# Kernel tuning notes

Hardware: AMD Instinct MI355X
Metric: run time of the kernel (lower is better)

## Reference

```python
import jax, jax.numpy as jnp
import numpy as np

NUM_FRAMES = 6
HEADS = 16
DIM_HEAD = 64


def setup_inputs() -> dict:
    key = jax.random.key(0)
    ks = jax.random.split(key, 7)
    D = 1024
    x = jax.random.normal(ks[0], (12, 1024, D), dtype=jnp.float32)
    context = jax.random.normal(ks[1], (2, 1024, D), dtype=jnp.float32)
    s = 1.0 / np.sqrt(D)
    Wq = jax.random.normal(ks[2], (D, D), dtype=jnp.float32) * s
    Wk = jax.random.normal(ks[3], (D, D), dtype=jnp.float32) * s
    Wv = jax.random.normal(ks[4], (D, D), dtype=jnp.float32) * s
    Wo = jax.random.normal(ks[5], (D, D), dtype=jnp.float32) * s
    bo = jnp.zeros((D,), dtype=jnp.float32)
    return {"x": x, "context": context, "Wq": Wq, "Wk": Wk, "Wv": Wv, "Wo": Wo, "bo": bo}


def reference(x, context, Wq, Wk, Wv, Wo, bo):
    B, S, D = x.shape  # B=12, S=1024, D=1024
    scale = DIM_HEAD ** (-0.5)
    ab = B // NUM_FRAMES  # actual batch after frame inflation
    xr = x.reshape(ab, NUM_FRAMES * S, D)  # [ab, 6144, D]
    # Linear projections (torch Linear: y = x @ W.T)
    q = xr @ Wq.T            # [ab, Sq, inner]
    k = context @ Wk.T       # [ab, Sk, inner]
    v = context @ Wv.T
    Sq = q.shape[1]
    Sk = k.shape[1]
    q = q.reshape(ab, Sq, HEADS, DIM_HEAD).transpose(0, 2, 1, 3)  # [ab,h,Sq,d]
    k = k.reshape(ab, Sk, HEADS, DIM_HEAD).transpose(0, 2, 1, 3)
    v = v.reshape(ab, Sk, HEADS, DIM_HEAD).transpose(0, 2, 1, 3)
    attn = jnp.einsum("bhqd,bhkd->bhqk", q, k) * scale
    attn = jax.nn.softmax(attn, axis=-1)
    out = jnp.einsum("bhqk,bhkd->bhqd", attn, v)
    out = out.transpose(0, 2, 1, 3).reshape(ab, Sq, HEADS * DIM_HEAD)
    out = out @ Wo.T + bo  # dropout is identity at p=0 / eval
    return out.reshape(B, S, D)
```

## Files before the change

kernel.cpp:

```cpp
#include <hip/hip_runtime.h>

typedef short bf16x8 __attribute__((ext_vector_type(8)));
typedef float floatx4 __attribute__((ext_vector_type(4)));
typedef unsigned short u16;
typedef unsigned int u32;

__device__ __forceinline__ u16 f2bf(float f) {
  u32 u = __float_as_uint(f);
  u += 0x7FFF + ((u >> 16) & 1);
  return (u16)(u >> 16);
}
__device__ __forceinline__ u32 packbf(float a, float b) {
  return (u32)f2bf(a) | ((u32)f2bf(b) << 16);
}
__device__ __forceinline__ u32 permpack(u32 a_bits, u32 b_bits) {
  return __builtin_amdgcn_perm(b_bits, a_bits, 0x07060302u);
}

__device__ __forceinline__ float ex2(float x) {
#if __has_builtin(__builtin_amdgcn_exp2f)
  return __builtin_amdgcn_exp2f(x);
#else
  float r;
  asm("v_exp_f32 %0, %1" : "=v"(r) : "v"(x));
  return r;
#endif
}

__device__ __forceinline__ void gload_lds16(const u16* g, u16* l) {
  __builtin_amdgcn_global_load_lds(
      (const __attribute__((address_space(1))) void*)(const void*)g,
      (__attribute__((address_space(3))) void*)(void*)l, 16, 0, 0);
}

__device__ __forceinline__ int xcd_swz(int disp, int nwg) {
  const int q = nwg >> 3;
  return (disp & 7) * q + (disp >> 3);
}

__device__ __forceinline__ void bb_mainloop(const u16* __restrict__ A,
                                            const u16* __restrict__ W,
                                            u16* As, u16* Ws, int m0, int n0,
                                            floatx4 acc[4][4]) {
  const int tid = threadIdx.x, lane = tid & 63, w = tid >> 6;
  const int wm = w & 1, wn = w >> 1;
  const int m16 = lane & 15, quad = lane >> 4;
  const int lr = lane >> 2;
  const int sc = (lane & 3) * 8;

  const u16* Ag = A + (size_t)(m0 + w * 32 + lr) * 1024 + sc;
  const u16* Wg = W + (size_t)(n0 + w * 32 + lr) * 1024 + sc;
  u16* const Asl = &As[(w * 32) * 32];
  u16* const Wsl = &Ws[(w * 32) * 32];

#pragma unroll
  for (int i = 0; i < 4; ++i)
#pragma unroll
    for (int j = 0; j < 4; ++j) acc[i][j] = (floatx4)0.0f;

  for (int kt = 0; kt < 32; ++kt) {
    gload_lds16(Ag, Asl);
    gload_lds16(Ag + 16 * 1024, Asl + 16 * 32);
    gload_lds16(Wg, Wsl);
    gload_lds16(Wg + 16 * 1024, Wsl + 16 * 32);
    Ag += 32;
    Wg += 32;
    __syncthreads();
    bf16x8 af[4], bfr[4];
#pragma unroll
    for (int t = 0; t < 4; ++t) {
      af[t]  = *(const bf16x8*)&As[(wm * 64 + t * 16 + m16) * 32 + quad * 8];
      bfr[t] = *(const bf16x8*)&Ws[(wn * 64 + t * 16 + m16) * 32 + quad * 8];
    }
#pragma unroll
    for (int i = 0; i < 4; ++i)
#pragma unroll
      for (int j = 0; j < 4; ++j)
        acc[i][j] = __builtin_amdgcn_mfma_f32_16x16x32_bf16(af[i], bfr[j],
                                                            acc[i][j], 0, 0, 0);
    __syncthreads();
  }
}

__global__ __launch_bounds__(256) void gemm_qkv(
    const u16* __restrict__ xb, const u16* __restrict__ ctxb,
    const u16* __restrict__ wqb, const u16* __restrict__ wkb,
    const u16* __restrict__ wvb, u16* __restrict__ Qb, u16* __restrict__ Kbuf,
    u16* __restrict__ Vtb) {
  __shared__ u16 As[128 * 32];
  __shared__ u16 Ws[128 * 32];
  const int lane = threadIdx.x & 63, w = threadIdx.x >> 6;
  const int wm = w & 1, wn = w >> 1;
  const int m16 = lane & 15, quad = lane >> 4;
  const int disp = blockIdx.y * 8 + blockIdx.x;
  const int work = xcd_swz(disp, 1024);
  const int y = work >> 3;
  const int n0 = (work & 7) * 128;
  const u16 *A, *W;
  int m0, mode;
  if (y < 96)       { A = xb;   W = wqb; m0 = y * 128;         mode = 0; }
  else if (y < 112) { A = ctxb; W = wkb; m0 = (y - 96) * 128;  mode = 1; }
  else              { A = ctxb; W = wvb; m0 = (y - 112) * 128; mode = 2; }
  floatx4 acc[4][4];
  bb_mainloop(A, W, As, Ws, m0, n0, acc);
  const float cs = (mode == 0) ? 0.18033688011112042f : 1.0f;
#pragma unroll
  for (int j = 0; j < 4; ++j) {
    const int col = n0 + wn * 64 + j * 16 + m16;
#pragma unroll
    for (int i = 0; i < 4; ++i)
#pragma unroll
      for (int r = 0; r < 4; ++r) {
        const int row = m0 + wm * 64 + i * 16 + quad * 4 + r;
        const u16 v = f2bf(acc[i][j][r] * cs);
        if (mode == 0)
          Qb[(size_t)row * 1024 + col] = v;
        else if (mode == 1)
          Kbuf[(size_t)row * 1024 + col] = v;
        else
          Vtb[((size_t)((row >> 10) * 1024 + col)) * 1024 + (row & 1023)] = v;
      }
  }
}

__global__ __launch_bounds__(256) void gemm_out(const u16* __restrict__ A,
                                                const u16* __restrict__ W,
                                                float* __restrict__ C,
                                                const float* __restrict__ bias) {
  __shared__ u16 As[128 * 32];
  __shared__ u16 Ws[128 * 32];
  const int lane = threadIdx.x & 63, w = threadIdx.x >> 6;
  const int wm = w & 1, wn = w >> 1;
  const int m16 = lane & 15, quad = lane >> 4;
  const int disp = blockIdx.y * 8 + blockIdx.x;
  const int work = xcd_swz(disp, 768);
  const int n0 = (work & 7) * 128, m0 = (work >> 3) * 128;
  floatx4 acc[4][4];
  bb_mainloop(A, W, As, Ws, m0, n0, acc);
#pragma unroll
  for (int j = 0; j < 4; ++j) {
    const int col = n0 + wn * 64 + j * 16 + m16;
    const float bv = bias[col];
#pragma unroll
    for (int i = 0; i < 4; ++i)
#pragma unroll
      for (int r = 0; r < 4; ++r) {
        const int row = m0 + wm * 64 + i * 16 + quad * 4 + r;
        C[(size_t)row * 1024 + col] = acc[i][j][r] + bv;
      }
  }
}

__global__ __launch_bounds__(256) void cvt_all(
    const float* __restrict__ x, const float* __restrict__ ctx,
    const float* __restrict__ wq, const float* __restrict__ wk,
    const float* __restrict__ wv, const float* __restrict__ wo,
    u16* __restrict__ xb, u16* __restrict__ ctxb, u16* __restrict__ wqb,
    u16* __restrict__ wkb, u16* __restrict__ wvb, u16* __restrict__ wob) {
  const u32 i = blockIdx.x * 256 + threadIdx.x;
  const float* s;
  u16* d;
  u32 o;
  if (i < 3145728u)      { s = x;   d = xb;   o = i; }
  else if (i < 3670016u) { s = ctx; d = ctxb; o = i - 3145728u; }
  else if (i < 3932160u) { s = wq;  d = wqb;  o = i - 3670016u; }
  else if (i < 4194304u) { s = wk;  d = wkb;  o = i - 3932160u; }
  else if (i < 4456448u) { s = wv;  d = wvb;  o = i - 4194304u; }
  else                   { s = wo;  d = wob;  o = i - 4456448u; }
  const float4 v = ((const float4*)s)[o];
  uint2 p;
  p.x = packbf(v.x, v.y);
  p.y = packbf(v.z, v.w);
  ((uint2*)d)[o] = p;
}

__global__ __launch_bounds__(256, 4) void attn_flash(
    const u16* __restrict__ Q, const u16* __restrict__ Kb,
    const u16* __restrict__ Vt, u16* __restrict__ O) {
  __shared__ u16 Kl[2 * 64 * 32];
  __shared__ u16 Vl[2 * 64 * 32];
  __shared__ u32 Pl[4 * 32 * 36];
  const int tid = threadIdx.x, lane = tid & 63, w = tid >> 6;
  const int m16 = lane & 15, quad = lane >> 4;
  const int disp =
      blockIdx.x + 48 * (blockIdx.y + 16 * blockIdx.z);
  const int work = xcd_swz(disp, 1536);
  const int qx = work % 48;
  const int bh = work / 48;
  const int h = bh & 15, b = bh >> 4;
  const int q0 = qx * 128 + w * 32;
  u32* const pbase = &Pl[w * 32 * 36];

  bf16x8 aq[2][2];
#pragma unroll
  for (int qt = 0; qt < 2; ++qt)
#pragma unroll
    for (int ks = 0; ks < 2; ++ks)
      aq[qt][ks] =
          *(const bf16x8*)&Q[((size_t)(b * 6144 + q0 + qt * 16 + m16)) * 1024 +
                             h * 64 + ks * 32 + quad * 8];

  const int wk = w & 1, wh = w >> 1;
  const u16* kg = Kb + ((size_t)(b * 1024 + wh * 32 + (lane >> 2))) * 1024 +
                  h * 64 + wk * 32 + (lane & 3) * 8;
  const u16* vg = Vt + ((size_t)(b * 16 + h)) * 65536 +
                  (size_t)(wh * 32 + (lane >> 2)) * 1024 + wk * 32 +
                  (lane & 3) * 8;
  u16* const klb = &Kl[wk * 2048 + wh * 1024];
  u16* const vlb = &Vl[wk * 2048 + wh * 1024];

  bf16x8 vone;
#pragma unroll
  for (int e = 0; e < 8; ++e) vone[e] = (short)0x3F80;

  floatx4 oacc[2][4];
#pragma unroll
  for (int qt = 0; qt < 2; ++qt)
#pragma unroll
    for (int mtd = 0; mtd < 4; ++mtd) oacc[qt][mtd] = (floatx4)0.0f;
  floatx4 lacc[2];
  lacc[0] = (floatx4)0.0f;
  lacc[1] = (floatx4)0.0f;

#pragma unroll 1
  for (int kt = 0; kt < 16; ++kt) {
    gload_lds16(kg, klb);
    gload_lds16(kg + 16 * 1024, klb + 512);
    gload_lds16(vg, vlb);
    gload_lds16(vg + 16 * 1024, vlb + 512);
    kg += 64 * 1024;
    vg += 64;
    __syncthreads();

    floatx4 sst[2][4];
#pragma unroll
    for (int mt = 0; mt < 4; ++mt) {
      const int row = mt * 16 + m16;
      const bf16x8 kf0 = *(const bf16x8*)&Kl[row * 32 + quad * 8];
      const bf16x8 kf1 = *(const bf16x8*)&Kl[2048 + row * 32 + quad * 8];
#pragma unroll
      for (int qt = 0; qt < 2; ++qt) {
        floatx4 t = (floatx4)0.0f;
        t = __builtin_amdgcn_mfma_f32_16x16x32_bf16(kf0, aq[qt][0], t, 0, 0, 0);
        sst[qt][mt] =
            __builtin_amdgcn_mfma_f32_16x16x32_bf16(kf1, aq[qt][1], t, 0, 0, 0);
      }
    }
#pragma unroll
    for (int qt = 0; qt < 2; ++qt) {
      u32* const prow = &pbase[(qt * 16 + m16) * 36 + quad * 2];
#pragma unroll
      for (int mt = 0; mt < 4; ++mt) {
        const u32 b0 = __float_as_uint(ex2(sst[qt][mt][0]));
        const u32 b1 = __float_as_uint(ex2(sst[qt][mt][1]));
        const u32 b2 = __float_as_uint(ex2(sst[qt][mt][2]));
        const u32 b3 = __float_as_uint(ex2(sst[qt][mt][3]));
        uint2 pk;
        pk.x = permpack(b0, b1);
        pk.y = permpack(b2, b3);
        *(uint2*)&prow[mt * 8] = pk;
      }
    }
#pragma unroll
    for (int kk = 0; kk < 2; ++kk) {
      bf16x8 pf[2];
#pragma unroll
      for (int qt = 0; qt < 2; ++qt)
        pf[qt] =
            *(const bf16x8*)&pbase[(qt * 16 + m16) * 36 + kk * 16 + quad * 4];
      lacc[0] = __builtin_amdgcn_mfma_f32_16x16x32_bf16(vone, pf[0], lacc[0],
                                                        0, 0, 0);
      lacc[1] = __builtin_amdgcn_mfma_f32_16x16x32_bf16(vone, pf[1], lacc[1],
                                                        0, 0, 0);
#pragma unroll
      for (int mtd = 0; mtd < 4; ++mtd) {
        const bf16x8 vf =
            *(const bf16x8*)&Vl[kk * 2048 + (mtd * 16 + m16) * 32 + quad * 8];
#pragma unroll
        for (int qt = 0; qt < 2; ++qt)
          oacc[qt][mtd] = __builtin_amdgcn_mfma_f32_16x16x32_bf16(
              vf, pf[qt], oacc[qt][mtd], 0, 0, 0);
      }
    }
    __syncthreads();
  }

#pragma unroll
  for (int qt = 0; qt < 2; ++qt) {
    const float linv = 1.0f / lacc[qt][0];
    const size_t obase =
        ((size_t)(b * 6144 + q0 + qt * 16 + m16)) * 1024 + h * 64;
#pragma unroll
    for (int mtd = 0; mtd < 4; ++mtd) {
      const int d0 = mtd * 16 + quad * 4;
      *(u32*)&O[obase + d0] =
          packbf(oacc[qt][mtd][0] * linv, oacc[qt][mtd][1] * linv);
      *(u32*)&O[obase + d0 + 2] =
          packbf(oacc[qt][mtd][2] * linv, oacc[qt][mtd][3] * linv);
    }
  }
}

template <bool A_BF16, bool OUT_F32, int VT, bool BIAS>
__global__ __launch_bounds__(256) void gemm_nt(
    const void* __restrict__ Ap, const float* __restrict__ W,
    void* __restrict__ Cp, const float* __restrict__ bias, int M, int N,
    int K, float scale) {
  __shared__ u16 As[128 * 40];
  __shared__ u16 Ws[128 * 40];
  const int tid = threadIdx.x;
  const int lane = tid & 63;
  const int wv = tid >> 6;
  const int wm = wv & 1, wn = wv >> 1;
  const int m16 = lane & 15, quad = lane >> 4;
  const int n0 = blockIdx.x * 128;
  const int m0 = blockIdx.y * 128;
  const int lr = tid >> 2;
  const int lc = (tid & 3) * 8;
  floatx4 acc[4][4];
#pragma unroll
  for (int i = 0; i < 4; ++i)
#pragma unroll
    for (int j = 0; j < 4; ++j) acc[i][j] = (floatx4)0.0f;
  const int KT = K >> 5;
  for (int kt = 0; kt < KT; ++kt) {
    const int k0 = kt << 5;
#pragma unroll
    for (int j = 0; j < 2; ++j) {
      const int r = lr + 64 * j;
      if (A_BF16) {
        *(uint4*)&As[r * 40 + lc] =
            *(const uint4*)&((const u16*)Ap)[(size_t)(m0 + r) * K + k0 + lc];
      } else {
        const float* Arow = (const float*)Ap + (size_t)(m0 + r) * K + k0 + lc;
        const float4 a0 = *(const float4*)Arow;
        const float4 a1 = *(const float4*)(Arow + 4);
        uint4 p;
        p.x = packbf(a0.x, a0.y); p.y = packbf(a0.z, a0.w);
        p.z = packbf(a1.x, a1.y); p.w = packbf(a1.z, a1.w);
        *(uint4*)&As[r * 40 + lc] = p;
      }
      const float* Wrow = W + (size_t)(n0 + r) * K + k0 + lc;
      const float4 w0 = *(const float4*)Wrow;
      const float4 w1 = *(const float4*)(Wrow + 4);
      uint4 q;
      q.x = packbf(w0.x, w0.y); q.y = packbf(w0.z, w0.w);
      q.z = packbf(w1.x, w1.y); q.w = packbf(w1.z, w1.w);
      *(uint4*)&Ws[r * 40 + lc] = q;
    }
    __syncthreads();
    bf16x8 af[4], bfr[4];
#pragma unroll
    for (int t = 0; t < 4; ++t) {
      af[t]  = *(const bf16x8*)&As[(wm * 64 + t * 16 + m16) * 40 + quad * 8];
      bfr[t] = *(const bf16x8*)&Ws[(wn * 64 + t * 16 + m16) * 40 + quad * 8];
    }
#pragma unroll
    for (int i = 0; i < 4; ++i)
#pragma unroll
      for (int j = 0; j < 4; ++j)
        acc[i][j] = __builtin_amdgcn_mfma_f32_16x16x32_bf16(af[i], bfr[j],
                                                            acc[i][j], 0, 0, 0);
    __syncthreads();
  }
#pragma unroll
  for (int j = 0; j < 4; ++j) {
    const int col = n0 + wn * 64 + j * 16 + m16;
    const float bv = BIAS ? bias[col] : 0.0f;
#pragma unroll
    for (int i = 0; i < 4; ++i)
#pragma unroll
      for (int r = 0; r < 4; ++r) {
        const int row = m0 + wm * 64 + i * 16 + quad * 4 + r;
        const float v = acc[i][j][r] * scale + bv;
        if (OUT_F32)
          ((float*)Cp)[(size_t)row * N + col] = v;
        else if (VT)
          ((u16*)Cp)[((size_t)((row >> 10) * 1024 + col)) * 1024 +
                     (row & 1023)] = f2bf(v);
        else
          ((u16*)Cp)[(size_t)row * N + col] = f2bf(v);
      }
  }
}

extern "C" void kernel_launch(void* const* d_in, const int* in_sizes, int n_in,
                              void* d_out, int out_size, void* d_ws,
                              size_t ws_size, hipStream_t stream) {
  const float* x   = (const float*)d_in[0];
  const float* ctx = (const float*)d_in[1];
  const float* Wq  = (const float*)d_in[2];
  const float* Wk  = (const float*)d_in[3];
  const float* Wv  = (const float*)d_in[4];
  const float* Wo  = (const float*)d_in[5];
  const float* bo  = (const float*)d_in[6];
  float* out = (float*)d_out;
  const dim3 blk(256);
  const float CS = 0.18033688011112042f;

  u16* Qb   = (u16*)d_ws;
  u16* Kbuf = Qb + 12582912;
  u16* Vtb  = Kbuf + 2097152;
  u16* Obx  = Vtb + 2097152;
  u16* ctxb = Obx + 12582912;
  u16* wqb  = ctxb + 2097152;
  u16* wkb  = wqb + 1048576;
  u16* wvb  = wkb + 1048576;
  u16* wob  = wvb + 1048576;
  const size_t need = (size_t)(wob + 1048576 - Qb) * sizeof(u16);

  if (ws_size >= need) {
    cvt_all<<<18432, blk, 0, stream>>>(x, ctx, Wq, Wk, Wv, Wo, Obx, ctxb, wqb,
                                       wkb, wvb, wob);
    gemm_qkv<<<dim3(8, 128), blk, 0, stream>>>(Obx, ctxb, wqb, wkb, wvb, Qb,
                                               Kbuf, Vtb);
    attn_flash<<<dim3(48, 16, 2), blk, 0, stream>>>(Qb, Kbuf, Vtb, Obx);
    gemm_out<<<dim3(8, 96), blk, 0, stream>>>(Obx, wob, out, bo);
  } else {
    gemm_nt<false, false, 0, false><<<dim3(8, 96), blk, 0, stream>>>(
        x, Wq, Qb, nullptr, 12288, 1024, 1024, CS);
    gemm_nt<false, false, 0, false><<<dim3(8, 16), blk, 0, stream>>>(
        ctx, Wk, Kbuf, nullptr, 2048, 1024, 1024, 1.0f);
    gemm_nt<false, false, 1, false><<<dim3(8, 16), blk, 0, stream>>>(
        ctx, Wv, Vtb, nullptr, 2048, 1024, 1024, 1.0f);
    attn_flash<<<dim3(48, 16, 2), blk, 0, stream>>>(Qb, Kbuf, Vtb, Obx);
    gemm_nt<true, true, 0, true><<<dim3(8, 96), blk, 0, stream>>>(
        Obx, Wo, out, bo, 12288, 1024, 1024, 1.0f);
  }
}
```

Measured before the change: 287.7 us.

## Double GEMM K-tile to 64, add occupancy hint, vectorize V-transpose stores

The shared bf16 GEMM main loop now stages a K=64 slice per iteration, as two 32-wide LDS halves, so it runs half as many iterations and half as many barrier pairs. Both GEMM kernels get launch_bounds(256,4) to hint the register budget for four blocks per CU. The transposed V store in the QKV epilogue writes four packed bf16 values as one 8-byte store instead of four scalar stores. LDS per block doubles to 32 KB, which may limit occupancy, and the loop is still not double-buffered.

Measured after the change: 257.1 us. 1.12x faster.

```diff
diff --git a/kernel.cpp b/kernel.cpp
--- a/kernel.cpp
+++ b/kernel.cpp
@@ -38,10 +38,30 @@
   return (disp & 7) * q + (disp >> 3);
 }
 
-__device__ __forceinline__ void bb_mainloop(const u16* __restrict__ A,
-                                            const u16* __restrict__ W,
-                                            u16* As, u16* Ws, int m0, int n0,
-                                            floatx4 acc[4][4]) {
+__device__ __forceinline__ void bb_frags(const u16* As, const u16* Ws, int wm,
+                                         int wn, int m16, int quad,
+                                         bf16x8 af[4], bf16x8 bfr[4]) {
+#pragma unroll
+  for (int t = 0; t < 4; ++t) {
+    af[t]  = *(const bf16x8*)&As[(wm * 64 + t * 16 + m16) * 32 + quad * 8];
+    bfr[t] = *(const bf16x8*)&Ws[(wn * 64 + t * 16 + m16) * 32 + quad * 8];
+  }
+}
+
+__device__ __forceinline__ void bb_mfma(const bf16x8 af[4], const bf16x8 bfr[4],
+                                        floatx4 acc[4][4]) {
+#pragma unroll
+  for (int i = 0; i < 4; ++i)
+#pragma unroll
+    for (int j = 0; j < 4; ++j)
+      acc[i][j] = __builtin_amdgcn_mfma_f32_16x16x32_bf16(af[i], bfr[j],
+                                                          acc[i][j], 0, 0, 0);
+}
+
+__device__ __forceinline__ void bb_mainloop64(const u16* __restrict__ A,
+                                              const u16* __restrict__ W,
+                                              u16* As, u16* Ws, int m0, int n0,
+                                              floatx4 acc[4][4]) {
   const int tid = threadIdx.x, lane = tid & 63, w = tid >> 6;
   const int wm = w & 1, wn = w >> 1;
   const int m16 = lane & 15, quad = lane >> 4;
@@ -58,37 +78,34 @@
 #pragma unroll
     for (int j = 0; j < 4; ++j) acc[i][j] = (floatx4)0.0f;
 
-  for (int kt = 0; kt < 32; ++kt) {
+  for (int kt = 0; kt < 16; ++kt) {
     gload_lds16(Ag, Asl);
-    gload_lds16(Ag + 16 * 1024, Asl + 16 * 32);
+    gload_lds16(Ag + 16 * 1024, Asl + 512);
+    gload_lds16(Ag + 32, Asl + 4096);
+    gload_lds16(Ag + 32 + 16 * 1024, Asl + 4096 + 512);
     gload_lds16(Wg, Wsl);
-    gload_lds16(Wg + 16 * 1024, Wsl + 16 * 32);
-    Ag += 32;
-    Wg += 32;
+    gload_lds16(Wg + 16 * 1024, Wsl + 512);
+    gload_lds16(Wg + 32, Wsl + 4096);
+    gload_lds16(Wg + 32 + 16 * 1024, Wsl + 4096 + 512);
+    Ag += 64;
+    Wg += 64;
     __syncthreads();
     bf16x8 af[4], bfr[4];
-#pragma unroll
-    for (int t = 0; t < 4; ++t) {
-      af[t]  = *(const bf16x8*)&As[(wm * 64 + t * 16 + m16) * 32 + quad * 8];
-      bfr[t] = *(const bf16x8*)&Ws[(wn * 64 + t * 16 + m16) * 32 + quad * 8];
-    }
-#pragma unroll
-    for (int i = 0; i < 4; ++i)
-#pragma unroll
-      for (int j = 0; j < 4; ++j)
-        acc[i][j] = __builtin_amdgcn_mfma_f32_16x16x32_bf16(af[i], bfr[j],
-                                                            acc[i][j], 0, 0, 0);
-    __syncthreads();
-  }
-}
-
-__global__ __launch_bounds__(256) void gemm_qkv(
+    bb_frags(As, Ws, wm, wn, m16, quad, af, bfr);
+    bb_mfma(af, bfr, acc);
+    bb_frags(As + 4096, Ws + 4096, wm, wn, m16, quad, af, bfr);
+    bb_mfma(af, bfr, acc);
+    __syncthreads();
+  }
+}
+
+__global__ __launch_bounds__(256, 4) void gemm_qkv(
     const u16* __restrict__ xb, const u16* __restrict__ ctxb,
     const u16* __restrict__ wqb, const u16* __restrict__ wkb,
     const u16* __restrict__ wvb, u16* __restrict__ Qb, u16* __restrict__ Kbuf,
     u16* __restrict__ Vtb) {
-  __shared__ u16 As[128 * 32];
-  __shared__ u16 Ws[128 * 32];
+  __shared__ u16 As[128 * 64];
+  __shared__ u16 Ws[128 * 64];
   const int lane = threadIdx.x & 63, w = threadIdx.x >> 6;
   const int wm = w & 1, wn = w >> 1;
   const int m16 = lane & 15, quad = lane >> 4;
@@ -102,33 +119,41 @@
   else if (y < 112) { A = ctxb; W = wkb; m0 = (y - 96) * 128;  mode = 1; }
   else              { A = ctxb; W = wvb; m0 = (y - 112) * 128; mode = 2; }
   floatx4 acc[4][4];
-  bb_mainloop(A, W, As, Ws, m0, n0, acc);
+  bb_mainloop64(A, W, As, Ws, m0, n0, acc);
   const float cs = (mode == 0) ? 0.18033688011112042f : 1.0f;
 #pragma unroll
   for (int j = 0; j < 4; ++j) {
     const int col = n0 + wn * 64 + j * 16 + m16;
 #pragma unroll
-    for (int i = 0; i < 4; ++i)
-#pragma unroll
-      for (int r = 0; r < 4; ++r) {
-        const int row = m0 + wm * 64 + i * 16 + quad * 4 + r;
-        const u16 v = f2bf(acc[i][j][r] * cs);
-        if (mode == 0)
-          Qb[(size_t)row * 1024 + col] = v;
-        else if (mode == 1)
-          Kbuf[(size_t)row * 1024 + col] = v;
-        else
-          Vtb[((size_t)((row >> 10) * 1024 + col)) * 1024 + (row & 1023)] = v;
-      }
-  }
-}
-
-__global__ __launch_bounds__(256) void gemm_out(const u16* __restrict__ A,
-                                                const u16* __restrict__ W,
-                                                float* __restrict__ C,
-                                                const float* __restrict__ bias) {
-  __shared__ u16 As[128 * 32];
-  __shared__ u16 Ws[128 * 32];
+    for (int i = 0; i < 4; ++i) {
+      if (mode == 2) {
+        const int row0 = m0 + wm * 64 + i * 16 + quad * 4;
+        uint2 pv;
+        pv.x = packbf(acc[i][j][0], acc[i][j][1]);
+        pv.y = packbf(acc[i][j][2], acc[i][j][3]);
+        *(uint2*)&Vtb[((size_t)((row0 >> 10) * 1024 + col)) * 1024 +
+                      (row0 & 1023)] = pv;
+      } else {
+#pragma unroll
+        for (int r = 0; r < 4; ++r) {
+          const int row = m0 + wm * 64 + i * 16 + quad * 4 + r;
+          const u16 v = f2bf(acc[i][j][r] * cs);
+          if (mode == 0)
+            Qb[(size_t)row * 1024 + col] = v;
+          else
+            Kbuf[(size_t)row * 1024 + col] = v;
+        }
+      }
+    }
+  }
+}
+
+__global__ __launch_bounds__(256, 4) void gemm_out(const u16* __restrict__ A,
+                                                   const u16* __restrict__ W,
+                                                   float* __restrict__ C,
+                                                   const float* __restrict__ bias) {
+  __shared__ u16 As[128 * 64];
+  __shared__ u16 Ws[128 * 64];
   const int lane = threadIdx.x & 63, w = threadIdx.x >> 6;
   const int wm = w & 1, wn = w >> 1;
   const int m16 = lane & 15, quad = lane >> 4;
@@ -136,7 +161,7 @@
   const int work = xcd_swz(disp, 768);
   const int n0 = (work & 7) * 128, m0 = (work >> 3) * 128;
   floatx4 acc[4][4];
-  bb_mainloop(A, W, As, Ws, m0, n0, acc);
+  bb_mainloop64(A, W, As, Ws, m0, n0, acc);
 #pragma unroll
   for (int j = 0; j < 4; ++j) {
     const int col = n0 + wn * 64 + j * 16 + m16;
```
